# Optimization experiments

Hardware: AMD Instinct MI355X
Metric: run time of the kernel (lower is better)

## Reference

```python
import jax, jax.numpy as jnp
import numpy as np

B, S, H, L, NH = 8, 512, 768, 12, 8
DH = H // NH
FF = 4 * H
EPS = 1e-5


def setup_inputs() -> dict:
    key = jax.random.key(0)
    ks = iter(jax.random.split(key, 32))
    sc = 0.02
    rn = lambda shape: sc * jax.random.normal(next(ks), shape, dtype=jnp.float32)
    d = {}
    d["features"] = jax.random.normal(next(ks), (B, S, 20), dtype=jnp.float32)
    # feature encoder
    d["w_enc"] = rn((20, H)); d["b_enc"] = jnp.zeros((H,), jnp.float32)
    # transformer layers (stacked over L)
    d["wqkv"] = rn((L, H, 3 * H)); d["bqkv"] = jnp.zeros((L, 3 * H), jnp.float32)
    d["wo"] = rn((L, H, H)); d["bo"] = jnp.zeros((L, H), jnp.float32)
    d["ln1_g"] = jnp.ones((L, H), jnp.float32); d["ln1_b"] = jnp.zeros((L, H), jnp.float32)
    d["w1"] = rn((L, H, FF)); d["b1"] = jnp.zeros((L, FF), jnp.float32)
    d["w2"] = rn((L, FF, H)); d["b2"] = jnp.zeros((L, H), jnp.float32)
    d["ln2_g"] = jnp.ones((L, H), jnp.float32); d["ln2_b"] = jnp.zeros((L, H), jnp.float32)
    # heads
    d["wd1"] = rn((H, H)); d["bd1"] = jnp.zeros((H,), jnp.float32)
    d["wd2"] = rn((H, H)); d["bd2"] = jnp.zeros((H,), jnp.float32)
    d["wa1"] = rn((H, H)); d["ba1"] = jnp.zeros((H,), jnp.float32)
    d["wa2"] = rn((H, 3)); d["ba2"] = jnp.zeros((3,), jnp.float32)
    return d


def _layernorm(x, g, b):
    mu = jnp.mean(x, axis=-1, keepdims=True)
    var = jnp.mean(jnp.square(x - mu), axis=-1, keepdims=True)
    return (x - mu) * jax.lax.rsqrt(var + EPS) * g + b


def _build_coords(dist, ang):
    # dist: [S, H] (indexed dist[i, i-1] as in the original), ang: [S, 3]
    bond_len = jnp.float32(3.8)
    bond_ang = jnp.float32(np.deg2rad(120.0))
    c0 = jnp.zeros(3, jnp.float32)
    c1 = jnp.array([3.8, 0.0, 0.0], jnp.float32)
    c2 = jnp.array([3.8 + 3.8 * np.cos(np.deg2rad(120.0)),
                    3.8 * np.sin(np.deg2rad(120.0)), 0.0], jnp.float32)
    idx = jnp.arange(3, S)
    d1 = dist[idx, idx - 1]          # r
    psi = ang[idx, 1]                # theta
    omega = ang[idx, 2]              # chi

    def step(carry, inp):
        p1, p2, p3 = carry
        r, th, ch = inp
        e1 = p1 - p2
        e1 = e1 / jnp.linalg.norm(e1)
        u = p3 - p2
        u = u / jnp.linalg.norm(u)
        e3 = jnp.cross(e1, u)
        e3 = e3 / jnp.linalg.norm(e3)
        e2 = jnp.cross(e3, e1)
        pos = p1 + r * jnp.cos(th) * e1 \
              + r * jnp.sin(th) * jnp.cos(ch) * e2 \
              + r * jnp.sin(th) * jnp.sin(ch) * e3
        return (pos, p1, p2), pos

    _, rest = jax.lax.scan(step, (c2, c1, c0), (d1, psi, omega))
    return jnp.concatenate([jnp.stack([c0, c1, c2]), rest], axis=0)  # [S,3]


def _forward(features, w_enc, b_enc, wqkv, bqkv, wo, bo, ln1_g, ln1_b,
             w1, b1, w2, b2, ln2_g, ln2_b, wd1, bd1, wd2, bd2,
             wa1, ba1, wa2, ba2):
    hidden = jax.nn.relu(features @ w_enc + b_enc)  # [B,S,H]
    scale = 1.0 / jnp.sqrt(jnp.float32(DH))
    for l in range(L):
        qkv = hidden @ wqkv[l] + bqkv[l]            # [B,S,3H]
        q, k, v = jnp.split(qkv, 3, axis=-1)
        q = q.reshape(B, S, NH, DH)
        k = k.reshape(B, S, NH, DH)
        v = v.reshape(B, S, NH, DH)
        scores = jnp.einsum('bqhd,bkhd->bhqk', q, k) * scale
        attn = jax.nn.softmax(scores, axis=-1)
        ctx = jnp.einsum('bhqk,bkhd->bqhd', attn, v).reshape(B, S, H)
        attn_out = ctx @ wo[l] + bo[l]
        hidden = _layernorm(hidden + attn_out, ln1_g[l], ln1_b[l])
        ff = jax.nn.relu(hidden @ w1[l] + b1[l]) @ w2[l] + b2[l]
        hidden = _layernorm(hidden + ff, ln2_g[l], ln2_b[l])
    distances = jax.nn.relu(hidden @ wd1 + bd1) @ wd2 + bd2  # [B,S,H]
    angles = jax.nn.relu(hidden @ wa1 + ba1) @ wa2 + ba2     # [B,S,3]
    # original detaches before the coordinate build -> stop_gradient
    coords = jax.lax.stop_gradient(
        jax.vmap(_build_coords)(distances, angles))           # [B,S,3]
    return distances, angles, coords, hidden


def reference(features, w_enc, b_enc, wqkv, bqkv, wo, bo, ln1_g, ln1_b,
              w1, b1, w2, b2, ln2_g, ln2_b, wd1, bd1, wd2, bd2,
              wa1, ba1, wa2, ba2):
    return _forward(features, w_enc, b_enc, wqkv, bqkv, wo, bo, ln1_g, ln1_b,
                    w1, b1, w2, b2, ln2_g, ln2_b, wd1, bd1, wd2, bd2,
                    wa1, ba1, wa2, ba2)
```

## Files before the change

### kernel.cpp

```cpp
#include <hip/hip_runtime.h>
#include <math.h>

#define H 768
#define SEQ 512
#define BATCH 8
#define NHEADS 8
#define DHEAD 96
#define FFDIM 3072
#define NLAYERS 12
#define NTOK (BATCH*SEQ)

template<typename TA, typename TC, int ACT>
__global__ __launch_bounds__(256) void gemm_bias(
    const TA* __restrict__ A, const float* __restrict__ W,
    const float* __restrict__ bias, TC* __restrict__ C,
    int M, int N, int K)
{
    __shared__ double As[16][64];
    __shared__ double Bs[16][66];

    const int n0 = blockIdx.x * 64;
    const int m0 = blockIdx.y * 64;
    const int t  = threadIdx.x;

    const int arow = t >> 2, akq = t & 3;
    const int bk   = t >> 4, bnq = t & 15;
    const int tx   = t & 15, ty  = t >> 4;

    double acc[4][4] = {};
    const TA* Aptr = A + (size_t)(m0 + arow) * K + (akq << 2);
    const float* Wptr = W + (size_t)bk * N + n0 + (bnq << 2);

    for (int k0 = 0; k0 < K; k0 += 16) {
        #pragma unroll
        for (int j = 0; j < 4; ++j)
            As[(akq<<2)+j][arow] = (double)Aptr[k0 + j];
        #pragma unroll
        for (int j = 0; j < 4; ++j)
            Bs[bk][(bnq<<2)+j] = (double)Wptr[(size_t)k0 * N + j];
        __syncthreads();
        #pragma unroll
        for (int k = 0; k < 16; ++k) {
            double ar[4], br[4];
            #pragma unroll
            for (int i = 0; i < 4; ++i) ar[i] = As[k][(ty<<2)+i];
            #pragma unroll
            for (int j = 0; j < 4; ++j) br[j] = Bs[k][(tx<<2)+j];
            #pragma unroll
            for (int i = 0; i < 4; ++i)
                #pragma unroll
                for (int j = 0; j < 4; ++j)
                    acc[i][j] += ar[i] * br[j];
        }
        __syncthreads();
    }

    const float* bp = bias + n0 + (tx << 2);
    double bb[4] = {(double)bp[0], (double)bp[1], (double)bp[2], (double)bp[3]};
    #pragma unroll
    for (int i = 0; i < 4; ++i) {
        int row = m0 + (ty << 2) + i;
        #pragma unroll
        for (int j = 0; j < 4; ++j) {
            double v = acc[i][j] + bb[j];
            if (ACT) v = v > 0.0 ? v : 0.0;
            C[(size_t)row * N + n0 + (tx << 2) + j] = (TC)v;
        }
    }
}

__global__ __launch_bounds__(256) void encoder_kernel(
    const float* __restrict__ feats, const float* __restrict__ w,
    const float* __restrict__ b, double* __restrict__ out)
{
    __shared__ float f[20];
    const int row = blockIdx.x;
    const int t = threadIdx.x;
    if (t < 20) f[t] = feats[(size_t)row * 20 + t];
    __syncthreads();
    #pragma unroll
    for (int j = 0; j < 3; ++j) {
        int col = t + (j << 8);
        double s = (double)b[col];
        #pragma unroll
        for (int k = 0; k < 20; ++k) s += (double)f[k] * (double)w[k * H + col];
        out[(size_t)row * H + col] = s > 0.0 ? s : 0.0;
    }
}

__global__ __launch_bounds__(256) void attn_kernel(
    const float* __restrict__ qkv, float* __restrict__ ctx)
{
    const int bid = blockIdx.x;
    const int qt = bid & 31;
    const int h  = (bid >> 5) & 7;
    const int b  = bid >> 8;
    const int q0 = qt * 16;
    const int t  = threadIdx.x;

    __shared__ float Qs[16][96];
    __shared__ float KVs[32][100];
    __shared__ float Ss[16][512];

    const size_t base = ((size_t)b * SEQ) * (3 * H) + h * DHEAD;

    for (int i = t; i < 16 * 96; i += 256) {
        int r = i / 96, d = i % 96;
        Qs[r][d] = qkv[base + (size_t)(q0 + r) * (3 * H) + d];
    }
    __syncthreads();

    const int r  = t >> 4;
    const int kk = t & 15;
    const double scale = 0.10206207261596575;

    for (int kt = 0; kt < SEQ; kt += 32) {
        for (int i = t; i < 32 * 96; i += 256) {
            int rr = i / 96, d = i % 96;
            KVs[rr][d] = qkv[base + H + (size_t)(kt + rr) * (3 * H) + d];
        }
        __syncthreads();
        double s0 = 0.0, s1 = 0.0;
        #pragma unroll
        for (int d = 0; d < 96; d += 4) {
            float4 q4 = *(const float4*)&Qs[r][d];
            float4 k0 = *(const float4*)&KVs[kk][d];
            float4 k1 = *(const float4*)&KVs[kk + 16][d];
            s0 += (double)q4.x*(double)k0.x + (double)q4.y*(double)k0.y
                + (double)q4.z*(double)k0.z + (double)q4.w*(double)k0.w;
            s1 += (double)q4.x*(double)k1.x + (double)q4.y*(double)k1.y
                + (double)q4.z*(double)k1.z + (double)q4.w*(double)k1.w;
        }
        Ss[r][kt + kk]      = (float)(s0 * scale);
        Ss[r][kt + kk + 16] = (float)(s1 * scale);
        __syncthreads();
    }

    float mx = -1e30f;
    for (int j = 0; j < 32; ++j) mx = fmaxf(mx, Ss[r][kk + 16 * j]);
    #pragma unroll
    for (int o = 1; o < 16; o <<= 1) mx = fmaxf(mx, __shfl_xor(mx, o));
    double sum = 0.0;
    for (int j = 0; j < 32; ++j) {
        double e = exp((double)Ss[r][kk + 16 * j] - (double)mx);
        Ss[r][kk + 16 * j] = (float)e;
        sum += e;
    }
    #pragma unroll
    for (int o = 1; o < 16; o <<= 1) sum += __shfl_xor(sum, o);
    const double inv = 1.0 / sum;

    const int dd = kk * 6;
    double acc[6] = {};
    for (int kt = 0; kt < SEQ; kt += 32) {
        __syncthreads();
        for (int i = t; i < 32 * 96; i += 256) {
            int rr = i / 96, d = i % 96;
            KVs[rr][d] = qkv[base + 2 * H + (size_t)(kt + rr) * (3 * H) + d];
        }
        __syncthreads();
        for (int k = 0; k < 32; ++k) {
            double p = (double)Ss[r][kt + k];
            float2 v0 = *(const float2*)&KVs[k][dd];
            float2 v1 = *(const float2*)&KVs[k][dd + 2];
            float2 v2 = *(const float2*)&KVs[k][dd + 4];
            acc[0] += p * (double)v0.x; acc[1] += p * (double)v0.y;
            acc[2] += p * (double)v1.x; acc[3] += p * (double)v1.y;
            acc[4] += p * (double)v2.x; acc[5] += p * (double)v2.y;
        }
    }
    float* crow = ctx + ((size_t)(b * SEQ + q0 + r)) * H + h * DHEAD + dd;
    #pragma unroll
    for (int j = 0; j < 6; ++j) crow[j] = (float)(acc[j] * inv);
}

__global__ __launch_bounds__(256) void add_ln_kernel(
    double* __restrict__ hid, const double* __restrict__ x,
    const float* __restrict__ g, const float* __restrict__ bb)
{
    __shared__ double red[4];
    const int row = blockIdx.x;
    const int t = threadIdx.x;
    const size_t off = (size_t)row * H;

    double v[3]; double s = 0.0;
    #pragma unroll
    for (int j = 0; j < 3; ++j) {
        int c = t + (j << 8);
        v[j] = hid[off + c] + x[off + c];
        s += v[j];
    }
    #pragma unroll
    for (int o = 1; o < 64; o <<= 1) s += __shfl_xor(s, o);
    if ((t & 63) == 0) red[t >> 6] = s;
    __syncthreads();
    const double mu = (red[0] + red[1] + red[2] + red[3]) * (1.0 / H);
    __syncthreads();

    double q = 0.0;
    #pragma unroll
    for (int j = 0; j < 3; ++j) { double d = v[j] - mu; q += d * d; }
    #pragma unroll
    for (int o = 1; o < 64; o <<= 1) q += __shfl_xor(q, o);
    if ((t & 63) == 0) red[t >> 6] = q;
    __syncthreads();
    const double var = (red[0] + red[1] + red[2] + red[3]) * (1.0 / H);
    const double inv = 1.0 / sqrt(var + 1e-5);

    #pragma unroll
    for (int j = 0; j < 3; ++j) {
        int c = t + (j << 8);
        hid[off + c] = (v[j] - mu) * inv * (double)g[c] + (double)bb[c];
    }
}

__global__ __launch_bounds__(64) void angles_kernel(
    const float* __restrict__ T2, const float* __restrict__ wa2,
    const float* __restrict__ ba2, double* __restrict__ out)
{
    const int row = blockIdx.x;
    const int lane = threadIdx.x;
    const float* trow = T2 + (size_t)row * H;
    double p0 = 0.0, p1 = 0.0, p2 = 0.0;
    for (int d = lane; d < H; d += 64) {
        double v = (double)trow[d];
        p0 += v * (double)wa2[d * 3 + 0];
        p1 += v * (double)wa2[d * 3 + 1];
        p2 += v * (double)wa2[d * 3 + 2];
    }
    #pragma unroll
    for (int o = 1; o < 64; o <<= 1) {
        p0 += __shfl_xor(p0, o); p1 += __shfl_xor(p1, o); p2 += __shfl_xor(p2, o);
    }
    if (lane == 0) {
        out[(size_t)row * 3 + 0] = p0 + (double)ba2[0];
        out[(size_t)row * 3 + 1] = p1 + (double)ba2[1];
        out[(size_t)row * 3 + 2] = p2 + (double)ba2[2];
    }
}

__device__ __forceinline__ float cr_cosf(float x) { return (float)cos((double)x); }
__device__ __forceinline__ float cr_sinf(float x) { return (float)sin((double)x); }

__global__ void coords_kernel(const float* __restrict__ dist,
                              const float* __restrict__ ang,
                              float* __restrict__ out)
{
    const int b = threadIdx.x;
    if (b >= BATCH) return;

    const double ba = 2.0943951023931953;
    const float c2x = (float)(3.8 + 3.8 * cos(ba));
    const float c2y = (float)(3.8 * sin(ba));

    float p1[3] = {c2x, c2y, 0.f};
    float p2[3] = {3.8f, 0.f, 0.f};
    float p3[3] = {0.f, 0.f, 0.f};
    float* ob = out + (size_t)b * SEQ * 3;
    ob[0] = 0.f;  ob[1] = 0.f;  ob[2] = 0.f;
    ob[3] = 3.8f; ob[4] = 0.f;  ob[5] = 0.f;
    ob[6] = c2x;  ob[7] = c2y;  ob[8] = 0.f;

    for (int i = 3; i < SEQ; ++i) {
        float r  = dist[((size_t)(b * SEQ) + i) * H + (i - 1)];
        float th = ang[((size_t)(b * SEQ) + i) * 3 + 1];
        float ch = ang[((size_t)(b * SEQ) + i) * 3 + 2];

        float e1x = __fsub_rn(p1[0], p2[0]);
        float e1y = __fsub_rn(p1[1], p2[1]);
        float e1z = __fsub_rn(p1[2], p2[2]);
        float n = __fsqrt_rn(__fadd_rn(__fadd_rn(__fmul_rn(e1x, e1x),
                 __fmul_rn(e1y, e1y)), __fmul_rn(e1z, e1z)));
        e1x = __fdiv_rn(e1x, n); e1y = __fdiv_rn(e1y, n); e1z = __fdiv_rn(e1z, n);

        float ux = __fsub_rn(p3[0], p2[0]);
        float uy = __fsub_rn(p3[1], p2[1]);
        float uz = __fsub_rn(p3[2], p2[2]);
        n = __fsqrt_rn(__fadd_rn(__fadd_rn(__fmul_rn(ux, ux),
            __fmul_rn(uy, uy)), __fmul_rn(uz, uz)));
        ux = __fdiv_rn(ux, n); uy = __fdiv_rn(uy, n); uz = __fdiv_rn(uz, n);

        float e3x = __fsub_rn(__fmul_rn(e1y, uz), __fmul_rn(e1z, uy));
        float e3y = __fsub_rn(__fmul_rn(e1z, ux), __fmul_rn(e1x, uz));
        float e3z = __fsub_rn(__fmul_rn(e1x, uy), __fmul_rn(e1y, ux));
        n = __fsqrt_rn(__fadd_rn(__fadd_rn(__fmul_rn(e3x, e3x),
            __fmul_rn(e3y, e3y)), __fmul_rn(e3z, e3z)));
        e3x = __fdiv_rn(e3x, n); e3y = __fdiv_rn(e3y, n); e3z = __fdiv_rn(e3z, n);

        float e2x = __fsub_rn(__fmul_rn(e3y, e1z), __fmul_rn(e3z, e1y));
        float e2y = __fsub_rn(__fmul_rn(e3z, e1x), __fmul_rn(e3x, e1z));
        float e2z = __fsub_rn(__fmul_rn(e3x, e1y), __fmul_rn(e3y, e1x));

        float ct = cr_cosf(th), st = cr_sinf(th);
        float cc = cr_cosf(ch), sc = cr_sinf(ch);
        float A   = __fmul_rn(r, ct);
        float rst = __fmul_rn(r, st);
        float Bc  = __fmul_rn(rst, cc);
        float Cc  = __fmul_rn(rst, sc);

        float px = __fadd_rn(__fadd_rn(__fadd_rn(p1[0], __fmul_rn(A, e1x)),
                   __fmul_rn(Bc, e2x)), __fmul_rn(Cc, e3x));
        float py = __fadd_rn(__fadd_rn(__fadd_rn(p1[1], __fmul_rn(A, e1y)),
                   __fmul_rn(Bc, e2y)), __fmul_rn(Cc, e3y));
        float pz = __fadd_rn(__fadd_rn(__fadd_rn(p1[2], __fmul_rn(A, e1z)),
                   __fmul_rn(Bc, e2z)), __fmul_rn(Cc, e3z));

        float* op = ob + (size_t)i * 3;
        op[0] = px; op[1] = py; op[2] = pz;
        p3[0] = p2[0]; p3[1] = p2[1]; p3[2] = p2[2];
        p2[0] = p1[0]; p2[1] = p1[1]; p2[2] = p1[2];
        p1[0] = px;    p1[1] = py;    p1[2] = pz;
    }
}

__global__ void cast64to32_kernel(const double* __restrict__ src,
                                  float* __restrict__ dst, size_t n)
{
    size_t i = (size_t)blockIdx.x * blockDim.x + threadIdx.x;
    size_t stride = (size_t)gridDim.x * blockDim.x;
    for (; i < n; i += stride) dst[i] = (float)src[i];
}

extern "C" void kernel_launch(void* const* d_in, const int* in_sizes, int n_in,
                              void* d_out, int out_size, void* d_ws, size_t ws_size,
                              hipStream_t stream)
{
    const float* features = (const float*)d_in[0];
    const float* w_enc = (const float*)d_in[1];
    const float* b_enc = (const float*)d_in[2];
    const float* wqkv  = (const float*)d_in[3];
    const float* bqkv  = (const float*)d_in[4];
    const float* wo    = (const float*)d_in[5];
    const float* bo    = (const float*)d_in[6];
    const float* ln1_g = (const float*)d_in[7];
    const float* ln1_b = (const float*)d_in[8];
    const float* w1    = (const float*)d_in[9];
    const float* b1    = (const float*)d_in[10];
    const float* w2    = (const float*)d_in[11];
    const float* b2    = (const float*)d_in[12];
    const float* ln2_g = (const float*)d_in[13];
    const float* ln2_b = (const float*)d_in[14];
    const float* wd1   = (const float*)d_in[15];
    const float* bd1   = (const float*)d_in[16];
    const float* wd2   = (const float*)d_in[17];
    const float* bd2   = (const float*)d_in[18];
    const float* wa1   = (const float*)d_in[19];
    const float* ba1   = (const float*)d_in[20];
    const float* wa2   = (const float*)d_in[21];
    const float* ba2   = (const float*)d_in[22];

    char* wp = (char*)d_ws;
    double* hidden64 = (double*)wp;                       wp += (size_t)NTOK * H * 8;
    double* tmp64    = (double*)wp;                       wp += (size_t)NTOK * H * 8;
    double* dist64   = (double*)wp;                       wp += (size_t)NTOK * H * 8;
    double* ang64    = (double*)wp;                       wp += (size_t)NTOK * 3 * 8;
    float*  bigF     = (float*)wp;                        wp += (size_t)NTOK * FFDIM * 4;
    float*  ctxF     = (float*)wp;

    float* out_dist   = (float*)d_out;
    float* out_ang    = out_dist + (size_t)NTOK * H;
    float* out_coord  = out_ang + (size_t)NTOK * 3;
    float* out_hidden = out_coord + (size_t)NTOK * 3;

    encoder_kernel<<<NTOK, 256, 0, stream>>>(features, w_enc, b_enc, hidden64);

    for (int l = 0; l < NLAYERS; ++l) {
        gemm_bias<double, float, 0><<<dim3(3 * H / 64, NTOK / 64), 256, 0, stream>>>(
            hidden64, wqkv + (size_t)l * H * 3 * H, bqkv + (size_t)l * 3 * H,
            bigF, NTOK, 3 * H, H);
        attn_kernel<<<BATCH * NHEADS * (SEQ / 16), 256, 0, stream>>>(bigF, ctxF);
        gemm_bias<float, double, 0><<<dim3(H / 64, NTOK / 64), 256, 0, stream>>>(
            ctxF, wo + (size_t)l * H * H, bo + (size_t)l * H, tmp64, NTOK, H, H);
        add_ln_kernel<<<NTOK, 256, 0, stream>>>(hidden64, tmp64,
            ln1_g + (size_t)l * H, ln1_b + (size_t)l * H);
        gemm_bias<double, float, 1><<<dim3(FFDIM / 64, NTOK / 64), 256, 0, stream>>>(
            hidden64, w1 + (size_t)l * H * FFDIM, b1 + (size_t)l * FFDIM,
            bigF, NTOK, FFDIM, H);
        gemm_bias<float, double, 0><<<dim3(H / 64, NTOK / 64), 256, 0, stream>>>(
            bigF, w2 + (size_t)l * FFDIM * H, b2 + (size_t)l * H, tmp64, NTOK, H, FFDIM);
        add_ln_kernel<<<NTOK, 256, 0, stream>>>(hidden64, tmp64,
            ln2_g + (size_t)l * H, ln2_b + (size_t)l * H);
    }

    gemm_bias<double, float, 1><<<dim3(H / 64, NTOK / 64), 256, 0, stream>>>(
        hidden64, wd1, bd1, ctxF, NTOK, H, H);
    gemm_bias<float, double, 0><<<dim3(H / 64, NTOK / 64), 256, 0, stream>>>(
        ctxF, wd2, bd2, dist64, NTOK, H, H);
    gemm_bias<double, float, 1><<<dim3(H / 64, NTOK / 64), 256, 0, stream>>>(
        hidden64, wa1, ba1, ctxF, NTOK, H, H);
    angles_kernel<<<NTOK, 64, 0, stream>>>(ctxF, wa2, ba2, ang64);

    cast64to32_kernel<<<2048, 256, 0, stream>>>(dist64, out_dist, (size_t)NTOK * H);
    cast64to32_kernel<<<48, 256, 0, stream>>>(ang64, out_ang, (size_t)NTOK * 3);
    coords_kernel<<<1, 64, 0, stream>>>(out_dist, out_ang, out_coord);
    cast64to32_kernel<<<2048, 256, 0, stream>>>(hidden64, out_hidden, (size_t)NTOK * H);
}
```

Before: 26.20 ms.

## Enlarge FP64 GEMM tile to 128x64 with float weight staging and double attention smem

```diff
diff --git a/kernel.cpp b/kernel.cpp
--- a/kernel.cpp
+++ b/kernel.cpp
@@ -11,46 +11,59 @@
 #define NTOK (BATCH*SEQ)
 
 template<typename TA, typename TC, int ACT>
-__global__ __launch_bounds__(256) void gemm_bias(
+__global__ __launch_bounds__(256) void gemm64(
     const TA* __restrict__ A, const float* __restrict__ W,
     const float* __restrict__ bias, TC* __restrict__ C,
     int M, int N, int K)
 {
-    __shared__ double As[16][64];
-    __shared__ double Bs[16][66];
-
+    __shared__ double As[32][128];
+    __shared__ float  Bs[32][64];
+
+    const int m0 = blockIdx.y * 128;
     const int n0 = blockIdx.x * 64;
-    const int m0 = blockIdx.y * 64;
     const int t  = threadIdx.x;
-
-    const int arow = t >> 2, akq = t & 3;
-    const int bk   = t >> 4, bnq = t & 15;
-    const int tx   = t & 15, ty  = t >> 4;
-
-    double acc[4][4] = {};
-    const TA* Aptr = A + (size_t)(m0 + arow) * K + (akq << 2);
-    const float* Wptr = W + (size_t)bk * N + n0 + (bnq << 2);
-
-    for (int k0 = 0; k0 < K; k0 += 16) {
-        #pragma unroll
-        for (int j = 0; j < 4; ++j)
-            As[(akq<<2)+j][arow] = (double)Aptr[k0 + j];
-        #pragma unroll
-        for (int j = 0; j < 4; ++j)
-            Bs[bk][(bnq<<2)+j] = (double)Wptr[(size_t)k0 * N + j];
-        __syncthreads();
-        #pragma unroll
-        for (int k = 0; k < 16; ++k) {
-            double ar[4], br[4];
+    const int tx = t & 15;
+    const int ty = t >> 4;
+
+    const int arow = t >> 1;
+    const int kh   = (t & 1) << 4;
+    const TA* ap = A + (size_t)(m0 + arow) * K + kh;
+
+    const int bk  = t >> 4;
+    const int bnq = t & 15;
+
+    double acc[8][4];
+    #pragma unroll
+    for (int i = 0; i < 8; ++i)
+        #pragma unroll
+        for (int j = 0; j < 4; ++j) acc[i][j] = 0.0;
+
+    for (int k0 = 0; k0 < K; k0 += 32) {
+        #pragma unroll
+        for (int j = 0; j < 16; ++j)
+            As[kh + j][arow] = (double)ap[k0 + j];
+        *(float4*)&Bs[bk][bnq << 2] =
+            *(const float4*)(W + (size_t)(k0 + bk) * N + n0 + (bnq << 2));
+        *(float4*)&Bs[bk + 16][bnq << 2] =
+            *(const float4*)(W + (size_t)(k0 + bk + 16) * N + n0 + (bnq << 2));
+        __syncthreads();
+
+        #pragma unroll
+        for (int k = 0; k < 32; ++k) {
+            double ar[8];
             #pragma unroll
-            for (int i = 0; i < 4; ++i) ar[i] = As[k][(ty<<2)+i];
+            for (int j = 0; j < 4; ++j)
+                *(double2*)&ar[j << 1] = *(const double2*)&As[k][(ty << 3) + (j << 1)];
+            float4 bf = *(const float4*)&Bs[k][tx << 2];
+            double b0 = (double)bf.x, b1 = (double)bf.y;
+            double b2 = (double)bf.z, b3 = (double)bf.w;
             #pragma unroll
-            for (int j = 0; j < 4; ++j) br[j] = Bs[k][(tx<<2)+j];
-            #pragma unroll
-            for (int i = 0; i < 4; ++i)
-                #pragma unroll
-                for (int j = 0; j < 4; ++j)
-                    acc[i][j] += ar[i] * br[j];
+            for (int i = 0; i < 8; ++i) {
+                acc[i][0] = fma(ar[i], b0, acc[i][0]);
+                acc[i][1] = fma(ar[i], b1, acc[i][1]);
+                acc[i][2] = fma(ar[i], b2, acc[i][2]);
+                acc[i][3] = fma(ar[i], b3, acc[i][3]);
+            }
         }
         __syncthreads();
     }
@@ -58,8 +71,8 @@
     const float* bp = bias + n0 + (tx << 2);
     double bb[4] = {(double)bp[0], (double)bp[1], (double)bp[2], (double)bp[3]};
     #pragma unroll
-    for (int i = 0; i < 4; ++i) {
-        int row = m0 + (ty << 2) + i;
+    for (int i = 0; i < 8; ++i) {
+        int row = m0 + (ty << 3) + i;
         #pragma unroll
         for (int j = 0; j < 4; ++j) {
             double v = acc[i][j] + bb[j];
@@ -98,15 +111,15 @@
     const int q0 = qt * 16;
     const int t  = threadIdx.x;
 
-    __shared__ float Qs[16][96];
-    __shared__ float KVs[32][100];
-    __shared__ float Ss[16][512];
+    __shared__ double Qs[16][96];
+    __shared__ double KVs[32][100];
+    __shared__ float  Ss[16][512];
 
     const size_t base = ((size_t)b * SEQ) * (3 * H) + h * DHEAD;
 
     for (int i = t; i < 16 * 96; i += 256) {
         int r = i / 96, d = i % 96;
-        Qs[r][d] = qkv[base + (size_t)(q0 + r) * (3 * H) + d];
+        Qs[r][d] = (double)qkv[base + (size_t)(q0 + r) * (3 * H) + d];
     }
     __syncthreads();
 
@@ -117,19 +130,17 @@
     for (int kt = 0; kt < SEQ; kt += 32) {
         for (int i = t; i < 32 * 96; i += 256) {
             int rr = i / 96, d = i % 96;
-            KVs[rr][d] = qkv[base + H + (size_t)(kt + rr) * (3 * H) + d];
+            KVs[rr][d] = (double)qkv[base + H + (size_t)(kt + rr) * (3 * H) + d];
         }
         __syncthreads();
         double s0 = 0.0, s1 = 0.0;
         #pragma unroll
-        for (int d = 0; d < 96; d += 4) {
-            float4 q4 = *(const float4*)&Qs[r][d];
-            float4 k0 = *(const float4*)&KVs[kk][d];
-            float4 k1 = *(const float4*)&KVs[kk + 16][d];
-            s0 += (double)q4.x*(double)k0.x + (double)q4.y*(double)k0.y
-                + (double)q4.z*(double)k0.z + (double)q4.w*(double)k0.w;
-            s1 += (double)q4.x*(double)k1.x + (double)q4.y*(double)k1.y
-                + (double)q4.z*(double)k1.z + (double)q4.w*(double)k1.w;
+        for (int d = 0; d < 96; d += 2) {
+            double2 q  = *(const double2*)&Qs[r][d];
+            double2 ka = *(const double2*)&KVs[kk][d];
+            double2 kb = *(const double2*)&KVs[kk + 16][d];
+            s0 = fma(q.x, ka.x, s0); s0 = fma(q.y, ka.y, s0);
+            s1 = fma(q.x, kb.x, s1); s1 = fma(q.y, kb.y, s1);
         }
         Ss[r][kt + kk]      = (float)(s0 * scale);
         Ss[r][kt + kk + 16] = (float)(s1 * scale);
@@ -156,17 +167,17 @@
         __syncthreads();
         for (int i = t; i < 32 * 96; i += 256) {
             int rr = i / 96, d = i % 96;
-            KVs[rr][d] = qkv[base + 2 * H + (size_t)(kt + rr) * (3 * H) + d];
+            KVs[rr][d] = (double)qkv[base + 2 * H + (size_t)(kt + rr) * (3 * H) + d];
         }
         __syncthreads();
         for (int k = 0; k < 32; ++k) {
             double p = (double)Ss[r][kt + k];
-            float2 v0 = *(const float2*)&KVs[k][dd];
-            float2 v1 = *(const float2*)&KVs[k][dd + 2];
-            float2 v2 = *(const float2*)&KVs[k][dd + 4];
-            acc[0] += p * (double)v0.x; acc[1] += p * (double)v0.y;
-            acc[2] += p * (double)v1.x; acc[3] += p * (double)v1.y;
-            acc[4] += p * (double)v2.x; acc[5] += p * (double)v2.y;
+            double2 v0 = *(const double2*)&KVs[k][dd];
+            double2 v1 = *(const double2*)&KVs[k][dd + 2];
+            double2 v2 = *(const double2*)&KVs[k][dd + 4];
+            acc[0] = fma(p, v0.x, acc[0]); acc[1] = fma(p, v0.y, acc[1]);
+            acc[2] = fma(p, v1.x, acc[2]); acc[3] = fma(p, v1.y, acc[3]);
+            acc[4] = fma(p, v2.x, acc[4]); acc[5] = fma(p, v2.y, acc[5]);
         }
     }
     float* crow = ctx + ((size_t)(b * SEQ + q0 + r)) * H + h * DHEAD + dd;
@@ -365,28 +376,28 @@
     encoder_kernel<<<NTOK, 256, 0, stream>>>(features, w_enc, b_enc, hidden64);
 
     for (int l = 0; l < NLAYERS; ++l) {
-        gemm_bias<double, float, 0><<<dim3(3 * H / 64, NTOK / 64), 256, 0, stream>>>(
+        gemm64<double, float, 0><<<dim3(3 * H / 64, NTOK / 128), 256, 0, stream>>>(
             hidden64, wqkv + (size_t)l * H * 3 * H, bqkv + (size_t)l * 3 * H,
             bigF, NTOK, 3 * H, H);
         attn_kernel<<<BATCH * NHEADS * (SEQ / 16), 256, 0, stream>>>(bigF, ctxF);
-        gemm_bias<float, double, 0><<<dim3(H / 64, NTOK / 64), 256, 0, stream>>>(
+        gemm64<float, double, 0><<<dim3(H / 64, NTOK / 128), 256, 0, stream>>>(
             ctxF, wo + (size_t)l * H * H, bo + (size_t)l * H, tmp64, NTOK, H, H);
         add_ln_kernel<<<NTOK, 256, 0, stream>>>(hidden64, tmp64,
             ln1_g + (size_t)l * H, ln1_b + (size_t)l * H);
-        gemm_bias<double, float, 1><<<dim3(FFDIM / 64, NTOK / 64), 256, 0, stream>>>(
+        gemm64<double, float, 1><<<dim3(FFDIM / 64, NTOK / 128), 256, 0, stream>>>(
             hidden64, w1 + (size_t)l * H * FFDIM, b1 + (size_t)l * FFDIM,
             bigF, NTOK, FFDIM, H);
-        gemm_bias<float, double, 0><<<dim3(H / 64, NTOK / 64), 256, 0, stream>>>(
+        gemm64<float, double, 0><<<dim3(H / 64, NTOK / 128), 256, 0, stream>>>(
             bigF, w2 + (size_t)l * FFDIM * H, b2 + (size_t)l * H, tmp64, NTOK, H, FFDIM);
         add_ln_kernel<<<NTOK, 256, 0, stream>>>(hidden64, tmp64,
             ln2_g + (size_t)l * H, ln2_b + (size_t)l * H);
     }
 
-    gemm_bias<double, float, 1><<<dim3(H / 64, NTOK / 64), 256, 0, stream>>>(
+    gemm64<double, float, 1><<<dim3(H / 64, NTOK / 128), 256, 0, stream>>>(
         hidden64, wd1, bd1, ctxF, NTOK, H, H);
-    gemm_bias<float, double, 0><<<dim3(H / 64, NTOK / 64), 256, 0, stream>>>(
+    gemm64<float, double, 0><<<dim3(H / 64, NTOK / 128), 256, 0, stream>>>(
         ctxF, wd2, bd2, dist64, NTOK, H, H);
-    gemm_bias<double, float, 1><<<dim3(H / 64, NTOK / 64), 256, 0, stream>>>(
+    gemm64<double, float, 1><<<dim3(H / 64, NTOK / 128), 256, 0, stream>>>(
         hidden64, wa1, ba1, ctxF, NTOK, H, H);
     angles_kernel<<<NTOK, 64, 0, stream>>>(ctxF, wa2, ba2, ang64);
 
```

After: 27.61 ms. 5.4% more time.
